# Performance work log

Measured on AMD Instinct MI355X. Metric: run time of the kernel, lower is better.

## Reference

```python
import jax, jax.numpy as jnp
import numpy as np

H, HKV, D, HID, I, S = 32, 8, 128, 4096, 12288, 8192
EPS = 1e-6


def _rms(x, w):
    # RMSNorm over last dim (ANERMSNorm)
    return x * jax.lax.rsqrt(jnp.mean(x * x, axis=-1, keepdims=True) + EPS) * w


def _rotate_half(x):
    x1, x2 = jnp.split(x, 2, axis=-1)
    return jnp.concatenate([-x2, x1], axis=-1)


def setup_inputs() -> dict:
    key = jax.random.key(0)
    ks = jax.random.split(key, 12)
    std = 0.02
    pos = 1000.0
    # RoPE angles for this position (HF convention: emb = concat(freqs, freqs))
    inv_freq = 1.0 / (10000.0 ** (np.arange(0, D, 2, dtype=np.float32) / D))
    ang = np.concatenate([pos * inv_freq, pos * inv_freq])  # (D,)
    return {
        "hidden_conv": jax.random.normal(ks[0], (1, HID, 1, 1), jnp.float32),
        "position": jnp.array([pos], jnp.float32),
        "cos": jnp.asarray(np.cos(ang), jnp.float32).reshape(1, 1, D),
        "sin": jnp.asarray(np.sin(ang), jnp.float32).reshape(1, 1, D),
        "k_cache": jax.random.normal(ks[1], (1, HKV, S, D), jnp.float32),
        "v_cache": jax.random.normal(ks[2], (1, HKV, S, D), jnp.float32),
        "Wq": jax.random.normal(ks[3], (H * D, HID), jnp.float32) * std,
        "Wk": jax.random.normal(ks[4], (HKV * D, HID), jnp.float32) * std,
        "Wv": jax.random.normal(ks[5], (HKV * D, HID), jnp.float32) * std,
        "Wo": jax.random.normal(ks[6], (HID, H * D), jnp.float32) * std,
        "Wg": jax.random.normal(ks[7], (I, HID), jnp.float32) * std,
        "Wu": jax.random.normal(ks[8], (I, HID), jnp.float32) * std,
        "Wd": jax.random.normal(ks[9], (HID, I), jnp.float32) * std,
        "q_norm_w": jnp.ones((D,), jnp.float32),
        "k_norm_w": jnp.ones((D,), jnp.float32),
        "ln1_w": jnp.ones((HID,), jnp.float32),
        "ln2_w": jnp.ones((HID,), jnp.float32),
    }


def reference(hidden_conv, position, cos, sin, k_cache, v_cache,
              Wq, Wk, Wv, Wo, Wg, Wu, Wd,
              q_norm_w, k_norm_w, ln1_w, ln2_w):
    x = hidden_conv.reshape(HID)                      # conv layout -> vector
    residual = x
    h = _rms(x, ln1_w)
    # 1x1 conv projections == GEMV
    q = (Wq @ h).reshape(H, D)
    k = (Wk @ h).reshape(HKV, D)
    v = (Wv @ h).reshape(HKV, D)
    q = _rms(q, q_norm_w)
    k = _rms(k, k_norm_w)
    c, s = cos.reshape(D), sin.reshape(D)
    q = q * c + _rotate_half(q) * s
    k = k * c + _rotate_half(k) * s
    # mask-based KV cache write (scatter-free, as in original)
    pos = position.reshape(())
    positions = jnp.arange(S, dtype=jnp.float32)
    wmask = (positions == pos)[None, :, None]          # (1, S, 1)
    k_new = jnp.where(wmask, k[:, None, :], k_cache[0])  # (HKV, S, D)
    v_new = jnp.where(wmask, v[:, None, :], v_cache[0])
    # GQA repeat
    rep = H // HKV
    k_rep = jnp.repeat(k_new, rep, axis=0)             # (H, S, D)
    v_rep = jnp.repeat(v_new, rep, axis=0)
    scale = D ** -0.5
    scores = jnp.einsum('hd,hsd->hs', q, k_rep) * scale
    causal = jnp.where(positions > pos, jnp.float32(-10000.0), jnp.float32(0.0))
    attn = jax.nn.softmax(scores + causal, axis=-1)
    out = jnp.einsum('hs,hsd->hd', attn, v_rep).reshape(H * D)
    h1 = residual + Wo @ out
    # SwiGLU MLP
    h2 = _rms(h1, ln2_w)
    mlp = Wd @ (jax.nn.silu(Wg @ h2) * (Wu @ h2))
    hid = h1 + mlp
    return (hid.reshape(1, HID, 1, 1), k_new[None], v_new[None])
```

## Files before the change

kernel.cpp:

```cpp
#include <hip/hip_runtime.h>
#include <cstdint>
#include <cmath>

#define H 32
#define HKV 8
#define DD 128
#define HID 4096
#define II 12288
#define SS 8192
#define EPSF 1e-6f
#define CS 256
#define NC (SS / CS)

typedef float f4 __attribute__((ext_vector_type(4)));

__device__ __forceinline__ float wave_reduce_sum(float v) {
#pragma unroll
    for (int off = 32; off; off >>= 1) v += __shfl_down(v, off, 64);
    return v;
}

__device__ __forceinline__ f4 ntload(const f4* p) {
    return __builtin_nontemporal_load(p);
}

__global__ __launch_bounds__(256) void kv_bulk(const float* __restrict__ kc,
                                               const float* __restrict__ vc,
                                               float* __restrict__ ok,
                                               float* __restrict__ ov) {
    const f4* src = (blockIdx.y == 0) ? (const f4*)kc : (const f4*)vc;
    f4* dst = (blockIdx.y == 0) ? (f4*)ok : (f4*)ov;
    size_t base = (size_t)blockIdx.x * 1024 + threadIdx.x;
#pragma unroll
    for (int j = 0; j < 4; j++) {
        size_t i = base + (size_t)j * 256;
        __builtin_nontemporal_store(ntload(src + i), dst + i);
    }
}

__global__ __launch_bounds__(256) void gemv_qkv(const float* __restrict__ Wq,
                                                const float* __restrict__ Wk,
                                                const float* __restrict__ Wv,
                                                const float* __restrict__ x,
                                                const float* __restrict__ ln1,
                                                float* __restrict__ q,
                                                float* __restrict__ k,
                                                float* __restrict__ v) {
    __shared__ float red[4];
    int t = threadIdx.x;
    int wave = t >> 6, lane = t & 63;
    const f4* x4 = (const f4*)x;
    const f4* l4 = (const f4*)ln1;
    float ss = 0.f;
#pragma unroll
    for (int i = 0; i < 4; i++) {
        f4 a = x4[t + i * 256];
        ss += a.x * a.x + a.y * a.y + a.z * a.z + a.w * a.w;
    }
    ss = wave_reduce_sum(ss);
    if (lane == 0) red[wave] = ss;
    __syncthreads();
    float r = rsqrtf((red[0] + red[1] + red[2] + red[3]) * (1.f / (float)HID) + EPSF);

    int row = blockIdx.x * 4 + wave;
    const float* wrow;
    float* out;
    int ro;
    if (row < 4096)      { wrow = Wq + (size_t)row * HID;          out = q; ro = row; }
    else if (row < 5120) { wrow = Wk + (size_t)(row - 4096) * HID; out = k; ro = row - 4096; }
    else                 { wrow = Wv + (size_t)(row - 5120) * HID; out = v; ro = row - 5120; }
    const f4* w4 = (const f4*)wrow;
    float acc = 0.f;
#pragma unroll
    for (int ii = 0; ii < 16; ii++) {
        int i = lane + ii * 64;
        f4 a = ntload(w4 + i);
        f4 b = x4[i];
        f4 c = l4[i];
        acc += a.x * b.x * c.x + a.y * b.y * c.y + a.z * b.z * c.z + a.w * b.w * c.w;
    }
    acc = wave_reduce_sum(acc);
    if (lane == 0) out[ro] = acc * r;
}

__global__ __launch_bounds__(128) void rope_insert(float* __restrict__ q,
                                                   const float* __restrict__ k,
                                                   const float* __restrict__ v,
                                                   const float* __restrict__ cv,
                                                   const float* __restrict__ sv,
                                                   const float* __restrict__ qw,
                                                   const float* __restrict__ kw,
                                                   const float* __restrict__ position,
                                                   float* __restrict__ ok,
                                                   float* __restrict__ ov) {
    int b = blockIdx.x, t = threadIdx.x;
    int pos = (int)position[0];
    if (b >= 40) {
        int hv = b - 40;
        ov[((size_t)hv * SS + pos) * DD + t] = v[hv * DD + t];
        return;
    }
    bool isq = (b < H);
    const float* vec = isq ? (q + (size_t)b * DD) : (k + (size_t)(b - H) * DD);
    const float* nw = isq ? qw : kw;
    __shared__ float sh[DD];
    __shared__ float red[DD];
    float val = vec[t];
    red[t] = val * val;
    __syncthreads();
#pragma unroll
    for (int off = 64; off; off >>= 1) {
        if (t < off) red[t] += red[t + off];
        __syncthreads();
    }
    float r = rsqrtf(red[0] * (1.f / (float)DD) + EPSF);
    float nv = val * r * nw[t];
    sh[t] = nv;
    __syncthreads();
    float other = (t < 64) ? -sh[t + 64] : sh[t - 64];
    float res = nv * cv[t] + other * sv[t];
    if (isq) {
        q[(size_t)b * DD + t] = res;
    } else {
        int hk = b - H;
        ok[((size_t)hk * SS + pos) * DD + t] = res;
    }
}

__global__ __launch_bounds__(256) void attn_partial(const float* __restrict__ q,
                                                    const float* __restrict__ ok,
                                                    const float* __restrict__ ov,
                                                    const float* __restrict__ position,
                                                    float* __restrict__ pm,
                                                    float* __restrict__ pl,
                                                    float* __restrict__ po) {
    int h = blockIdx.x, c = blockIdx.y, t = threadIdx.x;
    int kvh = h >> 2;
    int pos = (int)position[0];
    if (c * CS > pos) {
        if (t == 0) { pm[h * NC + c] = -INFINITY; pl[h * NC + c] = 0.f; }
        return;
    }
    __shared__ float qs[DD];
    __shared__ float red[CS];
    __shared__ float pv[CS];
    if (t < DD) qs[t] = q[h * DD + t];
    __syncthreads();
    int s = c * CS + t;
    float score = -INFINITY;
    if (s <= pos) {
        const f4* kr = (const f4*)(ok + ((size_t)kvh * SS + s) * DD);
        const f4* q4 = (const f4*)qs;
        float acc = 0.f;
#pragma unroll
        for (int i = 0; i < DD / 4; i++) {
            f4 a = kr[i], b = q4[i];
            acc += a.x * b.x + a.y * b.y + a.z * b.z + a.w * b.w;
        }
        score = acc * 0.08838834764831845f;
    }
    red[t] = score;
    __syncthreads();
#pragma unroll
    for (int off = 128; off; off >>= 1) {
        if (t < off) red[t] = fmaxf(red[t], red[t + off]);
        __syncthreads();
    }
    float m = red[0];
    __syncthreads();
    float p = (score == -INFINITY) ? 0.f : expf(score - m);
    pv[t] = p;
    red[t] = p;
    __syncthreads();
#pragma unroll
    for (int off = 128; off; off >>= 1) {
        if (t < off) red[t] += red[t + off];
        __syncthreads();
    }
    float l = red[0];
    int jend = pos + 1 - c * CS;
    if (jend > CS) jend = CS;
    if (t < DD) {
        float acc = 0.f;
        for (int j = 0; j < jend; j++) {
            acc += pv[j] * ov[((size_t)kvh * SS + (size_t)(c * CS + j)) * DD + t];
        }
        po[((size_t)h * NC + c) * DD + t] = acc;
    }
    if (t == 0) {
        pm[h * NC + c] = m;
        pl[h * NC + c] = l;
    }
}

__global__ __launch_bounds__(128) void attn_combine(const float* __restrict__ pm,
                                                    const float* __restrict__ pl,
                                                    const float* __restrict__ po,
                                                    float* __restrict__ ao) {
    int h = blockIdx.x, d = threadIdx.x;
    float M = -INFINITY;
    for (int c = 0; c < NC; c++) M = fmaxf(M, pm[h * NC + c]);
    float L = 0.f, acc = 0.f;
    for (int c = 0; c < NC; c++) {
        float mm = pm[h * NC + c];
        if (mm == -INFINITY) continue;
        float wgt = expf(mm - M);
        L += wgt * pl[h * NC + c];
        acc += wgt * po[((size_t)h * NC + c) * DD + d];
    }
    ao[h * DD + d] = acc / L;
}

__global__ __launch_bounds__(256) void gemv_wo(const float* __restrict__ W,
                                               const float* __restrict__ xin,
                                               const float* __restrict__ resid,
                                               float* __restrict__ out) {
    int wave = threadIdx.x >> 6, lane = threadIdx.x & 63;
    int row = blockIdx.x * 4 + wave;
    const f4* w4 = (const f4*)(W + (size_t)row * HID);
    const f4* x4 = (const f4*)xin;
    float acc = 0.f;
#pragma unroll
    for (int ii = 0; ii < 16; ii++) {
        int i = lane + ii * 64;
        f4 a = ntload(w4 + i);
        f4 b = x4[i];
        acc += a.x * b.x + a.y * b.y + a.z * b.z + a.w * b.w;
    }
    acc = wave_reduce_sum(acc);
    if (lane == 0) out[row] = resid[row] + acc;
}

__global__ __launch_bounds__(256) void gemv_gateup(const float* __restrict__ Wg,
                                                   const float* __restrict__ Wu,
                                                   const float* __restrict__ h1,
                                                   const float* __restrict__ ln2,
                                                   float* __restrict__ m) {
    __shared__ float red[4];
    int t = threadIdx.x;
    int wave = t >> 6, lane = t & 63;
    const f4* x4 = (const f4*)h1;
    const f4* l4 = (const f4*)ln2;
    float ss = 0.f;
#pragma unroll
    for (int i = 0; i < 4; i++) {
        f4 a = x4[t + i * 256];
        ss += a.x * a.x + a.y * a.y + a.z * a.z + a.w * a.w;
    }
    ss = wave_reduce_sum(ss);
    if (lane == 0) red[wave] = ss;
    __syncthreads();
    float r = rsqrtf((red[0] + red[1] + red[2] + red[3]) * (1.f / (float)HID) + EPSF);

    int row = blockIdx.x * 4 + wave;
    const f4* g4 = (const f4*)(Wg + (size_t)row * HID);
    const f4* u4 = (const f4*)(Wu + (size_t)row * HID);
    float accg = 0.f, accu = 0.f;
#pragma unroll
    for (int ii = 0; ii < 16; ii++) {
        int i = lane + ii * 64;
        f4 b = x4[i];
        f4 c = l4[i];
        f4 hb; hb.x = b.x * c.x; hb.y = b.y * c.y; hb.z = b.z * c.z; hb.w = b.w * c.w;
        f4 a = ntload(g4 + i);
        accg += a.x * hb.x + a.y * hb.y + a.z * hb.z + a.w * hb.w;
        f4 u = ntload(u4 + i);
        accu += u.x * hb.x + u.y * hb.y + u.z * hb.z + u.w * hb.w;
    }
    accg = wave_reduce_sum(accg);
    accu = wave_reduce_sum(accu);
    if (lane == 0) {
        float g = accg * r, uu = accu * r;
        m[row] = (g / (1.f + expf(-g))) * uu;
    }
}

__global__ __launch_bounds__(256) void gemv_down(const float* __restrict__ Wd,
                                                 const float* __restrict__ mi,
                                                 const float* __restrict__ h1,
                                                 float* __restrict__ out) {
    int wave = threadIdx.x >> 6, lane = threadIdx.x & 63;
    int row = blockIdx.x * 4 + wave;
    const f4* w4 = (const f4*)(Wd + (size_t)row * II);
    const f4* x4 = (const f4*)mi;
    float acc = 0.f;
    for (int o = 0; o < 3; o++) {
#pragma unroll
        for (int ii = 0; ii < 16; ii++) {
            int i = lane + (o * 16 + ii) * 64;
            f4 a = ntload(w4 + i);
            f4 b = x4[i];
            acc += a.x * b.x + a.y * b.y + a.z * b.z + a.w * b.w;
        }
    }
    acc = wave_reduce_sum(acc);
    if (lane == 0) out[row] = h1[row] + acc;
}

extern "C" void kernel_launch(void* const* d_in, const int* in_sizes, int n_in,
                              void* d_out, int out_size, void* d_ws, size_t ws_size,
                              hipStream_t stream) {
    const float* x        = (const float*)d_in[0];
    const float* position = (const float*)d_in[1];
    const float* cosv     = (const float*)d_in[2];
    const float* sinv     = (const float*)d_in[3];
    const float* k_cache  = (const float*)d_in[4];
    const float* v_cache  = (const float*)d_in[5];
    const float* Wq       = (const float*)d_in[6];
    const float* Wk       = (const float*)d_in[7];
    const float* Wv       = (const float*)d_in[8];
    const float* Wo       = (const float*)d_in[9];
    const float* Wg       = (const float*)d_in[10];
    const float* Wu       = (const float*)d_in[11];
    const float* Wd       = (const float*)d_in[12];
    const float* q_norm_w = (const float*)d_in[13];
    const float* k_norm_w = (const float*)d_in[14];
    const float* ln1_w    = (const float*)d_in[15];
    const float* ln2_w    = (const float*)d_in[16];

    float* out_hid = (float*)d_out;
    float* out_k   = out_hid + HID;
    float* out_v   = out_k + (size_t)HKV * SS * DD;

    float* ws = (float*)d_ws;
    float* q        = ws;
    float* k        = q + H * DD;
    float* v        = k + HKV * DD;
    float* attn_out = v + HKV * DD;
    float* h1       = attn_out + H * DD;
    float* mi       = h1 + HID;
    float* part_m   = mi + II;
    float* part_l   = part_m + H * NC;
    float* part_o   = part_l + H * NC;

    kv_bulk<<<dim3(2048, 2), 256, 0, stream>>>(k_cache, v_cache, out_k, out_v);
    gemv_qkv<<<1536, 256, 0, stream>>>(Wq, Wk, Wv, x, ln1_w, q, k, v);
    rope_insert<<<48, 128, 0, stream>>>(q, k, v, cosv, sinv, q_norm_w, k_norm_w,
                                        position, out_k, out_v);
    attn_partial<<<dim3(H, NC), 256, 0, stream>>>(q, out_k, out_v, position,
                                                  part_m, part_l, part_o);
    attn_combine<<<H, 128, 0, stream>>>(part_m, part_l, part_o, attn_out);
    gemv_wo<<<1024, 256, 0, stream>>>(Wo, attn_out, x, h1);
    gemv_gateup<<<3072, 256, 0, stream>>>(Wg, Wu, h1, ln2_w, mi);
    gemv_down<<<1024, 256, 0, stream>>>(Wd, mi, h1, out_hid);
}
```

Measured before the change: 692.4 us.

## Fuse KV copy into QKV GEMV kernel and fold RoPE/insert into attention

Merges the KV-cache bulk copy into the QKV GEMV launch as extra blocks, and moves q/k RMSNorm, RoPE and the new-token KV write into the attention partial kernel. The attention kernel takes the new token's K/V from shared memory instead of reading it back from global memory. This removes two kernel launches and the serialisation between them. The copy now uses plain loads and stores rather than nontemporal ones, and every attention block recomputes the q normalisation and RoPE.

```diff
diff --git a/kernel.cpp b/kernel.cpp
--- a/kernel.cpp
+++ b/kernel.cpp
@@ -24,30 +24,35 @@
     return __builtin_nontemporal_load(p);
 }
 
-__global__ __launch_bounds__(256) void kv_bulk(const float* __restrict__ kc,
-                                               const float* __restrict__ vc,
-                                               float* __restrict__ ok,
-                                               float* __restrict__ ov) {
-    const f4* src = (blockIdx.y == 0) ? (const f4*)kc : (const f4*)vc;
-    f4* dst = (blockIdx.y == 0) ? (f4*)ok : (f4*)ov;
-    size_t base = (size_t)blockIdx.x * 1024 + threadIdx.x;
-#pragma unroll
-    for (int j = 0; j < 4; j++) {
-        size_t i = base + (size_t)j * 256;
-        __builtin_nontemporal_store(ntload(src + i), dst + i);
-    }
-}
-
-__global__ __launch_bounds__(256) void gemv_qkv(const float* __restrict__ Wq,
-                                                const float* __restrict__ Wk,
-                                                const float* __restrict__ Wv,
-                                                const float* __restrict__ x,
-                                                const float* __restrict__ ln1,
-                                                float* __restrict__ q,
-                                                float* __restrict__ k,
-                                                float* __restrict__ v) {
+__global__ __launch_bounds__(256) void front(const float* __restrict__ Wq,
+                                             const float* __restrict__ Wk,
+                                             const float* __restrict__ Wv,
+                                             const float* __restrict__ x,
+                                             const float* __restrict__ ln1,
+                                             const float* __restrict__ kc,
+                                             const float* __restrict__ vc,
+                                             float* __restrict__ q,
+                                             float* __restrict__ k,
+                                             float* __restrict__ v,
+                                             float* __restrict__ ok,
+                                             float* __restrict__ ov) {
     __shared__ float red[4];
+    int b = blockIdx.x;
     int t = threadIdx.x;
+    if (b >= 1536) {
+        int idx = b - 1536;
+        const f4* src;
+        f4* dst;
+        if (idx < 2048) { src = (const f4*)kc; dst = (f4*)ok; }
+        else            { src = (const f4*)vc; dst = (f4*)ov; idx -= 2048; }
+        size_t base = (size_t)idx * 1024 + t;
+#pragma unroll
+        for (int j = 0; j < 4; j++) {
+            size_t i = base + (size_t)j * 256;
+            dst[i] = src[i];
+        }
+        return;
+    }
     int wave = t >> 6, lane = t & 63;
     const f4* x4 = (const f4*)x;
     const f4* l4 = (const f4*)ln1;
@@ -62,7 +67,7 @@
     __syncthreads();
     float r = rsqrtf((red[0] + red[1] + red[2] + red[3]) * (1.f / (float)HID) + EPSF);
 
-    int row = blockIdx.x * 4 + wave;
+    int row = b * 4 + wave;
     const float* wrow;
     float* out;
     int ro;
@@ -75,87 +80,93 @@
     for (int ii = 0; ii < 16; ii++) {
         int i = lane + ii * 64;
         f4 a = ntload(w4 + i);
-        f4 b = x4[i];
+        f4 b2 = x4[i];
         f4 c = l4[i];
-        acc += a.x * b.x * c.x + a.y * b.y * c.y + a.z * b.z * c.z + a.w * b.w * c.w;
+        acc += a.x * b2.x * c.x + a.y * b2.y * c.y + a.z * b2.z * c.z + a.w * b2.w * c.w;
     }
     acc = wave_reduce_sum(acc);
     if (lane == 0) out[ro] = acc * r;
 }
 
-__global__ __launch_bounds__(128) void rope_insert(float* __restrict__ q,
-                                                   const float* __restrict__ k,
-                                                   const float* __restrict__ v,
-                                                   const float* __restrict__ cv,
-                                                   const float* __restrict__ sv,
-                                                   const float* __restrict__ qw,
-                                                   const float* __restrict__ kw,
-                                                   const float* __restrict__ position,
-                                                   float* __restrict__ ok,
-                                                   float* __restrict__ ov) {
-    int b = blockIdx.x, t = threadIdx.x;
-    int pos = (int)position[0];
-    if (b >= 40) {
-        int hv = b - 40;
-        ov[((size_t)hv * SS + pos) * DD + t] = v[hv * DD + t];
-        return;
-    }
-    bool isq = (b < H);
-    const float* vec = isq ? (q + (size_t)b * DD) : (k + (size_t)(b - H) * DD);
-    const float* nw = isq ? qw : kw;
-    __shared__ float sh[DD];
-    __shared__ float red[DD];
-    float val = vec[t];
-    red[t] = val * val;
-    __syncthreads();
-#pragma unroll
-    for (int off = 64; off; off >>= 1) {
-        if (t < off) red[t] += red[t + off];
-        __syncthreads();
-    }
-    float r = rsqrtf(red[0] * (1.f / (float)DD) + EPSF);
-    float nv = val * r * nw[t];
-    sh[t] = nv;
-    __syncthreads();
-    float other = (t < 64) ? -sh[t + 64] : sh[t - 64];
-    float res = nv * cv[t] + other * sv[t];
-    if (isq) {
-        q[(size_t)b * DD + t] = res;
-    } else {
-        int hk = b - H;
-        ok[((size_t)hk * SS + pos) * DD + t] = res;
-    }
-}
-
-__global__ __launch_bounds__(256) void attn_partial(const float* __restrict__ q,
-                                                    const float* __restrict__ ok,
-                                                    const float* __restrict__ ov,
+__global__ __launch_bounds__(256) void attn_partial(const float* __restrict__ qraw,
+                                                    const float* __restrict__ kraw,
+                                                    const float* __restrict__ vraw,
+                                                    float* __restrict__ ok,
+                                                    float* __restrict__ ov,
+                                                    const float* __restrict__ cv,
+                                                    const float* __restrict__ sv,
+                                                    const float* __restrict__ qw,
+                                                    const float* __restrict__ kw,
                                                     const float* __restrict__ position,
                                                     float* __restrict__ pm,
                                                     float* __restrict__ pl,
                                                     float* __restrict__ po) {
     int h = blockIdx.x, c = blockIdx.y, t = threadIdx.x;
-    int kvh = h >> 2;
     int pos = (int)position[0];
     if (c * CS > pos) {
         if (t == 0) { pm[h * NC + c] = -INFINITY; pl[h * NC + c] = 0.f; }
         return;
     }
+    int kvh = h >> 2;
+    int pc = pos / CS;
+    bool haspos = (c == pc);
+
+    __shared__ float red[256];
+    __shared__ float sh[256];
     __shared__ float qs[DD];
-    __shared__ float red[CS];
-    __shared__ float pv[CS];
-    if (t < DD) qs[t] = q[h * DD + t];
-    __syncthreads();
+    __shared__ float ksh[DD];
+    __shared__ float vsh[DD];
+    __shared__ float pvs[CS];
+
+    float val = 0.f;
+    if (t < DD)            val = qraw[(size_t)h * DD + t];
+    else if (haspos)       val = kraw[(size_t)kvh * DD + (t - DD)];
+    red[t] = val * val;
+    __syncthreads();
+#pragma unroll
+    for (int off = 64; off; off >>= 1) {
+        if ((t & 127) < off) red[t] += red[t + off];
+        __syncthreads();
+    }
+    float rq = rsqrtf(red[0] * (1.f / (float)DD) + EPSF);
+    float rk = rsqrtf(red[DD] * (1.f / (float)DD) + EPSF);
+    if (t < DD)           sh[t] = val * rq * qw[t];
+    else if (haspos)      sh[t] = val * rk * kw[t - DD];
+    __syncthreads();
+    if (t < DD) {
+        float other = (t < 64) ? -sh[t + 64] : sh[t - 64];
+        qs[t] = sh[t] * cv[t] + other * sv[t];
+        if (haspos) vsh[t] = vraw[(size_t)kvh * DD + t];
+    } else if (haspos) {
+        int d = t - DD;
+        float other = (d < 64) ? -sh[DD + d + 64] : sh[DD + d - 64];
+        ksh[d] = sh[t] * cv[d] + other * sv[d];
+    }
+    __syncthreads();
+    if (haspos && (h & 3) == 0 && t < DD) {
+        ok[((size_t)kvh * SS + pos) * DD + t] = ksh[t];
+        ov[((size_t)kvh * SS + pos) * DD + t] = vsh[t];
+    }
+
     int s = c * CS + t;
     float score = -INFINITY;
     if (s <= pos) {
-        const f4* kr = (const f4*)(ok + ((size_t)kvh * SS + s) * DD);
         const f4* q4 = (const f4*)qs;
         float acc = 0.f;
-#pragma unroll
-        for (int i = 0; i < DD / 4; i++) {
-            f4 a = kr[i], b = q4[i];
-            acc += a.x * b.x + a.y * b.y + a.z * b.z + a.w * b.w;
+        if (s < pos) {
+            const f4* kr = (const f4*)(ok + ((size_t)kvh * SS + s) * DD);
+#pragma unroll
+            for (int i = 0; i < DD / 4; i++) {
+                f4 a = kr[i], bq = q4[i];
+                acc += a.x * bq.x + a.y * bq.y + a.z * bq.z + a.w * bq.w;
+            }
+        } else {
+            const f4* kr = (const f4*)ksh;
+#pragma unroll
+            for (int i = 0; i < DD / 4; i++) {
+                f4 a = kr[i], bq = q4[i];
+                acc += a.x * bq.x + a.y * bq.y + a.z * bq.z + a.w * bq.w;
+            }
         }
         score = acc * 0.08838834764831845f;
     }
@@ -169,7 +180,7 @@
     float m = red[0];
     __syncthreads();
     float p = (score == -INFINITY) ? 0.f : expf(score - m);
-    pv[t] = p;
+    pvs[t] = p;
     red[t] = p;
     __syncthreads();
 #pragma unroll
@@ -180,11 +191,13 @@
     float l = red[0];
     int jend = pos + 1 - c * CS;
     if (jend > CS) jend = CS;
+    int jlim = haspos ? jend - 1 : jend;
     if (t < DD) {
         float acc = 0.f;
-        for (int j = 0; j < jend; j++) {
-            acc += pv[j] * ov[((size_t)kvh * SS + (size_t)(c * CS + j)) * DD + t];
+        for (int j = 0; j < jlim; j++) {
+            acc += pvs[j] * ov[((size_t)kvh * SS + (size_t)(c * CS + j)) * DD + t];
         }
+        if (haspos) acc += pvs[jend - 1] * vsh[t];
         po[((size_t)h * NC + c) * DD + t] = acc;
     }
     if (t == 0) {
@@ -333,12 +346,11 @@
     float* part_l   = part_m + H * NC;
     float* part_o   = part_l + H * NC;
 
-    kv_bulk<<<dim3(2048, 2), 256, 0, stream>>>(k_cache, v_cache, out_k, out_v);
-    gemv_qkv<<<1536, 256, 0, stream>>>(Wq, Wk, Wv, x, ln1_w, q, k, v);
-    rope_insert<<<48, 128, 0, stream>>>(q, k, v, cosv, sinv, q_norm_w, k_norm_w,
-                                        position, out_k, out_v);
-    attn_partial<<<dim3(H, NC), 256, 0, stream>>>(q, out_k, out_v, position,
-                                                  part_m, part_l, part_o);
+    front<<<5632, 256, 0, stream>>>(Wq, Wk, Wv, x, ln1_w, k_cache, v_cache,
+                                    q, k, v, out_k, out_v);
+    attn_partial<<<dim3(H, NC), 256, 0, stream>>>(q, k, v, out_k, out_v,
+                                                  cosv, sinv, q_norm_w, k_norm_w,
+                                                  position, part_m, part_l, part_o);
     attn_combine<<<H, 128, 0, stream>>>(part_m, part_l, part_o, attn_out);
     gemv_wo<<<1024, 256, 0, stream>>>(Wo, attn_out, x, h1);
     gemv_gateup<<<3072, 256, 0, stream>>>(Wg, Wu, h1, ln2_w, mi);
```

Result: no change. 687.4 us (-0.7%).
